# Kernel optimization log

Hardware: AMD Instinct MI355X
Metric: run time of the kernel (lower is better)

Reference implementation:

```python
import jax, jax.numpy as jnp
import numpy as np

B, S, K, D = 2, 2048, 8, 1024
P, KP, DFF = 32, 4, 4096


def setup_inputs() -> dict:
    key = jax.random.key(0)
    ks = jax.random.split(key, 17)
    s = 0.02
    return {
        "x": jax.random.normal(ks[0], (B, S, D), jnp.float32),
        "router_out": jax.random.normal(ks[1], (B, S, D), jnp.float32),
        "topk_neuron_idx": jax.random.randint(ks[2], (B, S, K), 0, 512, jnp.int32),
        "topk_neuron_weights": jax.random.uniform(ks[3], (B, S, K), jnp.float32),
        "selected_neurons": jax.random.normal(ks[4], (B, S, K, D), jnp.float32),
        "context": jax.random.normal(ks[5], (B, S, D), jnp.float32),
        "Wq": jax.random.normal(ks[6], (D, D), jnp.float32) * s,
        "bq": jnp.zeros((D,), jnp.float32),
        "Wk": jax.random.normal(ks[7], (D, D), jnp.float32) * s,
        "bk": jnp.zeros((D,), jnp.float32),
        "Wv": jax.random.normal(ks[8], (D, D), jnp.float32) * s,
        "bv": jnp.zeros((D,), jnp.float32),
        "pattern_queries": jax.random.normal(ks[9], (P, D), jnp.float32) * s,
        "Wup": jax.random.normal(ks[10], (DFF, D), jnp.float32) * s,
        "bup": jnp.zeros((DFF,), jnp.float32),
        "Wdown": jax.random.normal(ks[11], (D, DFF), jnp.float32) * s,
        "bdown": jnp.zeros((D,), jnp.float32),
    }


def reference(x, router_out, topk_neuron_idx, topk_neuron_weights,
              selected_neurons, context, Wq, bq, Wk, bk, Wv, bv,
              pattern_queries, Wup, bup, Wdown, bdown):
    scale = 1.0 / jnp.sqrt(jnp.float32(D))
    # K-wide neuron self-attention (per token), torch Linear: y = x @ W.T + b
    q = jnp.einsum('bskd,ed->bske', selected_neurons, Wq) + bq
    kk = jnp.einsum('bskd,ed->bske', selected_neurons, Wk) + bk
    v = jnp.einsum('bskd,ed->bske', selected_neurons, Wv) + bv
    attn = jax.nn.softmax(jnp.einsum('bsqd,bskd->bsqk', q, kk) * scale, axis=-1)
    interacted = jnp.einsum('bsqk,bskd->bsqd', attn, v)  # [B,S,K,D]
    # pattern similarity: [B,S,P,K]
    nps = jnp.einsum('pd,bskd->bspk', pattern_queries, interacted) * scale
    neuron_based = (nps * topk_neuron_weights[:, :, None, :]).sum(-1)  # [B,S,P]
    context_based = jnp.einsum('bsd,pd->bsp', context, pattern_queries)
    pattern_scores = 0.5 * neuron_based + 0.5 * context_based
    topk_scores, topk_idx = jax.lax.top_k(pattern_scores, KP)  # [B,S,KP]
    topk_w = jax.nn.softmax(topk_scores, axis=-1)
    sel_attn = jnp.take_along_axis(nps, topk_idx[..., None], axis=2)  # [B,S,KP,K]
    final_attn = (topk_w[..., None] * jax.nn.softmax(sel_attn, axis=-1)).sum(2)  # [B,S,K]
    aggregated = jnp.einsum('bsk,bskd->bsd', final_attn, interacted)
    combined = x + aggregated
    h = jax.nn.gelu(combined @ Wup.T + bup, approximate=False)
    return h @ Wdown.T + bdown
```

## Files before the change

kernel.cpp:

```cpp
#include <hip/hip_runtime.h>
#include <math.h>

typedef unsigned short ushort_t;
typedef __attribute__((ext_vector_type(8))) short short8;
typedef __attribute__((ext_vector_type(4))) float floatx4;

static __device__ __forceinline__ ushort_t f2bf(float f){
  unsigned int u = __float_as_uint(f);
  unsigned int r = u + 0x7FFFu + ((u >> 16) & 1u);
  return (ushort_t)(r >> 16);
}
static __device__ __forceinline__ void unpack8(uint4 u, float* f){
  f[0] = __uint_as_float(u.x << 16); f[1] = __uint_as_float(u.x & 0xffff0000u);
  f[2] = __uint_as_float(u.y << 16); f[3] = __uint_as_float(u.y & 0xffff0000u);
  f[4] = __uint_as_float(u.z << 16); f[5] = __uint_as_float(u.z & 0xffff0000u);
  f[6] = __uint_as_float(u.w << 16); f[7] = __uint_as_float(u.w & 0xffff0000u);
}
static __device__ __forceinline__ uint4 pack8(const float* f){
  uint4 u;
  u.x = (unsigned)f2bf(f[0]) | ((unsigned)f2bf(f[1]) << 16);
  u.y = (unsigned)f2bf(f[2]) | ((unsigned)f2bf(f[3]) << 16);
  u.z = (unsigned)f2bf(f[4]) | ((unsigned)f2bf(f[5]) << 16);
  u.w = (unsigned)f2bf(f[6]) | ((unsigned)f2bf(f[7]) << 16);
  return u;
}

static __device__ __forceinline__ void gload16(const void* g, void* l){
  __builtin_amdgcn_global_load_lds((const __attribute__((address_space(1))) void*)g,
                                   (__attribute__((address_space(3))) void*)l, 16, 0, 0);
}

__global__ __launch_bounds__(256) void k_cvt_multi(
    const float* __restrict__ s0, ushort_t* __restrict__ d0, int e0,
    const float* __restrict__ s1, ushort_t* __restrict__ d1, int e1,
    const float* __restrict__ s2, ushort_t* __restrict__ d2, int e2,
    const float* __restrict__ s3, ushort_t* __restrict__ d3, int e3,
    const float* __restrict__ s4, ushort_t* __restrict__ d4, int e4,
    const float* __restrict__ s5, ushort_t* __restrict__ d5, int e5){
  int i = blockIdx.x * 256 + threadIdx.x;
  const float* s; ushort_t* d; int b;
  if      (i < e0){ s = s0; d = d0; b = 0;  }
  else if (i < e1){ s = s1; d = d1; b = e0; }
  else if (i < e2){ s = s2; d = d2; b = e1; }
  else if (i < e3){ s = s3; d = d3; b = e2; }
  else if (i < e4){ s = s4; d = d4; b = e3; }
  else if (i < e5){ s = s5; d = d5; b = e4; }
  else return;
  int j = i - b;
  float4 v = ((const float4*)s)[j];
  unsigned long long p = (unsigned long long)f2bf(v.x)
                       | ((unsigned long long)f2bf(v.y) << 16)
                       | ((unsigned long long)f2bf(v.z) << 32)
                       | ((unsigned long long)f2bf(v.w) << 48);
  ((unsigned long long*)d)[j] = p;
}

__global__ __launch_bounds__(256) void k_transpose3(const float* __restrict__ s0, ushort_t* __restrict__ d0,
                                                    const float* __restrict__ s1, ushort_t* __restrict__ d1,
                                                    const float* __restrict__ s2, ushort_t* __restrict__ d2){
  __shared__ float tile[32][33];
  const float* in; ushort_t* out;
  if      (blockIdx.z == 0){ in = s0; out = d0; }
  else if (blockIdx.z == 1){ in = s1; out = d1; }
  else                     { in = s2; out = d2; }
  int bx = blockIdx.x * 32, by = blockIdx.y * 32;
  int tx = threadIdx.x & 31, ty = threadIdx.x >> 5;
  for (int i = 0; i < 32; i += 8)
    tile[ty + i][tx] = in[(size_t)(by + ty + i) * 1024 + bx + tx];
  __syncthreads();
  for (int i = 0; i < 32; i += 8)
    out[(size_t)(bx + ty + i) * 1024 + by + tx] = f2bf(tile[tx][ty + i]);
}

__global__ __launch_bounds__(256) void k_prep(const float* __restrict__ bq,
                                              const ushort_t* __restrict__ WKT,
                                              float* __restrict__ wv,
                                              const float* __restrict__ pat,
                                              const float* __restrict__ bv,
                                              float* __restrict__ pb,
                                              const ushort_t* __restrict__ WVT,
                                              const ushort_t* __restrict__ PATB,
                                              ushort_t* __restrict__ PVB){
  const int bid = blockIdx.x;
  const int l = threadIdx.x & 63;
  if (bid < 256){
    int d = (bid << 2) + (threadIdx.x >> 6);
    const uint4* row = (const uint4*)(WKT + (size_t)d * 1024 + (l << 4));
    const float4* b4 = (const float4*)(bq + (l << 4));
    float w[16], bb[16];
    unpack8(row[0], w); unpack8(row[1], w + 8);
#pragma unroll
    for (int i = 0; i < 4; i++){
      float4 v = b4[i];
      bb[i*4] = v.x; bb[i*4+1] = v.y; bb[i*4+2] = v.z; bb[i*4+3] = v.w;
    }
    float a = 0.f;
#pragma unroll
    for (int i = 0; i < 16; i++) a += w[i] * bb[i];
#pragma unroll
    for (int s = 1; s < 64; s <<= 1) a += __shfl_xor(a, s);
    if (l == 0) wv[d] = a;
  } else if (bid < 264){
    int p = ((bid - 256) << 2) + (threadIdx.x >> 6);
    const float4* pr = (const float4*)(pat + p * 1024) + l;
    const float4* b4 = (const float4*)bv + l;
    float a = 0.f;
#pragma unroll
    for (int i = 0; i < 4; i++){
      float4 x = pr[i * 64], y = b4[i * 64];
      a += x.x * y.x + x.y * y.y + x.z * y.z + x.w * y.w;
    }
#pragma unroll
    for (int s = 1; s < 64; s <<= 1) a += __shfl_xor(a, s);
    if (l == 0) pb[p] = a;
  } else {
    int d = ((bid - 264) << 2) + (threadIdx.x >> 6);
    const uint4* wr = (const uint4*)(WVT + (size_t)d * 1024 + (l << 4));
    float w[16];
    unpack8(wr[0], w); unpack8(wr[1], w + 8);
    for (int p = 0; p < 32; p++){
      const uint4* pr = (const uint4*)(PATB + p * 1024 + (l << 4));
      float pw[16];
      unpack8(pr[0], pw); unpack8(pr[1], pw + 8);
      float a = 0.f;
#pragma unroll
      for (int i = 0; i < 16; i++) a += w[i] * pw[i];
#pragma unroll
      for (int s = 1; s < 64; s <<= 1) a += __shfl_xor(a, s);
      if (l == 0) PVB[p * 1024 + d] = f2bf(a);
    }
  }
}

template<int MODE, int GN>
__global__ __launch_bounds__(256) void k_gemm_bt(const ushort_t* __restrict__ A,
                                                 const ushort_t* __restrict__ B,
                                                 void* __restrict__ C,
                                                 const float* __restrict__ bias,
                                                 const float* __restrict__ Xadd,
                                                 int N, int K){
  __shared__ ushort_t As[128 * 32];
  __shared__ ushort_t Bs[128 * 32];
  const int tid = threadIdx.x;
  const int w = tid >> 6, l = tid & 63;
  const int id = blockIdx.x;
  const int xcd = id & 7;
  const int t2 = id >> 3;
  const int nt = t2 % GN;
  const int mt = ((t2 / GN) << 3) + xcd;
  const int m0 = mt << 7, n0 = nt << 7;
  const int wm = (w >> 1) << 6, wn = (w & 1) << 6;
  const int rA = (w << 4) + (l >> 2);
  const int cA = (l & 3) << 3;
  const int fr = l & 15, fq = l >> 4;

  floatx4 acc[4][4];
#pragma unroll
  for (int i = 0; i < 4; i++)
#pragma unroll
    for (int j = 0; j < 4; j++) acc[i][j] = (floatx4)0.0f;

  const ushort_t* Ab = A + (size_t)(m0 + rA) * K + cA;
  const ushort_t* Bb = B + (size_t)(n0 + rA) * K + cA;
  const size_t row64 = (size_t)64 * K;
  ushort_t* Asw = As + (w << 9);
  ushort_t* Bsw = Bs + (w << 9);

  for (int k0 = 0; k0 < K; k0 += 32){
    __syncthreads();
    gload16(Ab + k0, Asw);
    gload16(Ab + row64 + k0, Asw + 2048);
    gload16(Bb + k0, Bsw);
    gload16(Bb + row64 + k0, Bsw + 2048);
    __syncthreads();
    short8 af[4], bg[4];
#pragma unroll
    for (int i = 0; i < 4; i++){
      af[i] = *(const short8*)(As + ((wm + (i << 4) + fr) << 5) + (fq << 3));
      bg[i] = *(const short8*)(Bs + ((wn + (i << 4) + fr) << 5) + (fq << 3));
    }
#pragma unroll
    for (int i = 0; i < 4; i++)
#pragma unroll
      for (int j = 0; j < 4; j++)
        acc[i][j] = __builtin_amdgcn_mfma_f32_16x16x32_bf16(af[i], bg[j], acc[i][j], 0, 0, 0);
  }

#pragma unroll
  for (int i = 0; i < 4; i++){
    int row = m0 + wm + (i << 4) + (fq << 2);
#pragma unroll
    for (int j = 0; j < 4; j++){
      int col = n0 + wn + (j << 4) + fr;
      float b = (MODE >= 1) ? bias[col] : 0.0f;
#pragma unroll
      for (int r = 0; r < 4; r++){
        float v = acc[i][j][r] + b;
        size_t idx = (size_t)(row + r) * N + col;
        if (MODE == 2) v += Xadd[idx];
        if (MODE == 3) v = 0.5f * v * (1.0f + erff(v * 0.70710678118654752f));
        if (MODE == 4) ((float*)C)[idx] = v;
        else           ((ushort_t*)C)[idx] = f2bf(v);
      }
    }
  }
}

template<int MODE, int GN>
__global__ __launch_bounds__(256) void k_gemm_bt64(const ushort_t* __restrict__ A,
                                                   const ushort_t* __restrict__ B,
                                                   void* __restrict__ C,
                                                   const float* __restrict__ bias,
                                                   const float* __restrict__ Xadd,
                                                   int N, int K){
  __shared__ ushort_t As[64 * 32];
  __shared__ ushort_t Bs[128 * 32];
  const int tid = threadIdx.x;
  const int w = tid >> 6, l = tid & 63;
  const int id = blockIdx.x;
  const int xcd = id & 7;
  const int t2 = id >> 3;
  const int nt = t2 % GN;
  const int mt = ((t2 / GN) << 3) + xcd;
  const int m0 = mt << 6, n0 = nt << 7;
  const int wm = (w >> 1) << 5, wn = (w & 1) << 6;
  const int rA = (w << 4) + (l >> 2);
  const int cA = (l & 3) << 3;
  const int fr = l & 15, fq = l >> 4;

  floatx4 acc[2][4];
#pragma unroll
  for (int i = 0; i < 2; i++)
#pragma unroll
    for (int j = 0; j < 4; j++) acc[i][j] = (floatx4)0.0f;

  const ushort_t* Ab = A + (size_t)(m0 + rA) * K + cA;
  const ushort_t* Bb = B + (size_t)(n0 + rA) * K + cA;
  const size_t row64 = (size_t)64 * K;

  for (int k0 = 0; k0 < K; k0 += 32){
    __syncthreads();
    gload16(Ab + k0, As + (w << 9));
    gload16(Bb + k0, Bs + (w << 9));
    gload16(Bb + row64 + k0, Bs + 2048 + (w << 9));
    __syncthreads();
    short8 af[2], bg[4];
#pragma unroll
    for (int i = 0; i < 2; i++)
      af[i] = *(const short8*)(As + ((wm + (i << 4) + fr) << 5) + (fq << 3));
#pragma unroll
    for (int j = 0; j < 4; j++)
      bg[j] = *(const short8*)(Bs + ((wn + (j << 4) + fr) << 5) + (fq << 3));
#pragma unroll
    for (int i = 0; i < 2; i++)
#pragma unroll
      for (int j = 0; j < 4; j++)
        acc[i][j] = __builtin_amdgcn_mfma_f32_16x16x32_bf16(af[i], bg[j], acc[i][j], 0, 0, 0);
  }

#pragma unroll
  for (int i = 0; i < 2; i++){
    int row = m0 + wm + (i << 4) + (fq << 2);
#pragma unroll
    for (int j = 0; j < 4; j++){
      int col = n0 + wn + (j << 4) + fr;
      float b = (MODE >= 1) ? bias[col] : 0.0f;
#pragma unroll
      for (int r = 0; r < 4; r++){
        float v = acc[i][j][r] + b;
        size_t idx = (size_t)(row + r) * N + col;
        if (MODE == 2) v += Xadd[idx];
        if (MODE == 3) v = 0.5f * v * (1.0f + erff(v * 0.70710678118654752f));
        if (MODE == 4) ((float*)C)[idx] = v;
        else           ((ushort_t*)C)[idx] = f2bf(v);
      }
    }
  }
}

__global__ __launch_bounds__(256) void k_gemm_n32(const ushort_t* __restrict__ A,
                                                  const ushort_t* __restrict__ B,
                                                  float* __restrict__ C,
                                                  int K){
  __shared__ ushort_t As[128 * 32];
  __shared__ ushort_t Bs[32 * 32];
  const int tid = threadIdx.x;
  const int w = tid >> 6, l = tid & 63;
  const int m0 = blockIdx.x << 7;
  const int rA = (w << 4) + (l >> 2);
  const int cA = (l & 3) << 3;
  const int fr = l & 15, fq = l >> 4;

  floatx4 acc[2][2];
#pragma unroll
  for (int i = 0; i < 2; i++)
#pragma unroll
    for (int j = 0; j < 2; j++) acc[i][j] = (floatx4)0.0f;

  const ushort_t* Ab = A + (size_t)(m0 + rA) * K + cA;
  const ushort_t* Bb = B + (size_t)rA * K + cA;
  const size_t row64 = (size_t)64 * K;

  for (int k0 = 0; k0 < K; k0 += 32){
    __syncthreads();
    gload16(Ab + k0, As + (w << 9));
    gload16(Ab + row64 + k0, As + 2048 + (w << 9));
    if (w < 2) gload16(Bb + k0, Bs + (w << 9));
    __syncthreads();
    short8 af[2], bg[2];
#pragma unroll
    for (int i = 0; i < 2; i++)
      af[i] = *(const short8*)(As + (((w << 5) + (i << 4) + fr) << 5) + (fq << 3));
#pragma unroll
    for (int j = 0; j < 2; j++)
      bg[j] = *(const short8*)(Bs + (((j << 4) + fr) << 5) + (fq << 3));
#pragma unroll
    for (int i = 0; i < 2; i++)
#pragma unroll
      for (int j = 0; j < 2; j++)
        acc[i][j] = __builtin_amdgcn_mfma_f32_16x16x32_bf16(af[i], bg[j], acc[i][j], 0, 0, 0);
  }

#pragma unroll
  for (int i = 0; i < 2; i++){
    int row = m0 + (w << 5) + (i << 4) + (fq << 2);
#pragma unroll
    for (int j = 0; j < 2; j++){
      int col = (j << 4) + fr;
#pragma unroll
      for (int r = 0; r < 4; r++)
        C[(size_t)(row + r) * 32 + col] = acc[i][j][r];
    }
  }
}

__global__ __launch_bounds__(256) void k_attn(const ushort_t* __restrict__ T,
                                              const ushort_t* __restrict__ SNB,
                                              const ushort_t* __restrict__ PVB,
                                              const float* __restrict__ PBv,
                                              const float* __restrict__ CB,
                                              const float* __restrict__ TW,
                                              ushort_t* __restrict__ GSN){
  __shared__ float logit_s[4 * 256];
  __shared__ float attn_s[8 * 64];
  __shared__ float npr_s[8 * 256];
  __shared__ float nps_s[8 * 256];
  __shared__ float sc_s[8 * 32];
  __shared__ float tw_s[8 * 8];
  __shared__ float pb_s[32];
  __shared__ int   sel_s[8 * 4];
  __shared__ float tkw_s[8 * 4], rmax_s[8 * 4], rsum_s[8 * 4], fa_s[8 * 8], g_s[8 * 8];

  const int t = threadIdx.x;
  const int w = t >> 6, l = t & 63;
  const int tok0 = blockIdx.x << 3;
  const int pair = (blockIdx.x << 2) + w;

  {
    const size_t rbase = (size_t)pair * 16 + (l & 15);
    const int ko = (l >> 4) << 3;
    const ushort_t* Ap = T   + rbase * 1024 + ko;
    const ushort_t* Bp = SNB + rbase * 1024 + ko;
    const ushort_t* P0 = PVB + (size_t)(l & 15) * 1024 + ko;
    const ushort_t* P1 = P0 + 16 * 1024;
    floatx4 aL = (floatx4)0.0f, aP0 = (floatx4)0.0f, aP1 = (floatx4)0.0f;
#pragma unroll 4
    for (int k0 = 0; k0 < 1024; k0 += 32){
      short8 b = *(const short8*)(Bp + k0);
      aL  = __builtin_amdgcn_mfma_f32_16x16x32_bf16(*(const short8*)(Ap + k0), b, aL, 0, 0, 0);
      aP0 = __builtin_amdgcn_mfma_f32_16x16x32_bf16(*(const short8*)(P0 + k0), b, aP0, 0, 0, 0);
      aP1 = __builtin_amdgcn_mfma_f32_16x16x32_bf16(*(const short8*)(P1 + k0), b, aP1, 0, 0, 0);
    }
    const int col = l & 15, r0 = (l >> 4) << 2;
#pragma unroll
    for (int r = 0; r < 4; r++)
      logit_s[(w << 8) + (r0 + r) * 16 + col] = aL[r] * 0.03125f;
    const int tokloc = (w << 1) + (col >> 3), kk = col & 7;
#pragma unroll
    for (int r = 0; r < 4; r++){
      npr_s[(tokloc << 8) + kk * 32 + (r0 + r)]      = aP0[r];
      npr_s[(tokloc << 8) + kk * 32 + (r0 + r) + 16] = aP1[r];
    }
  }
  if (t < 64) tw_s[t] = TW[(tok0 << 3) + t];
  if (t < 32) pb_s[t] = PBv[t];
  __syncthreads();

  const int loc = t >> 5, q = t & 31;
  if (q < 8){
    const float* lrow = logit_s + ((loc >> 1) << 8) + (loc & 1) * 136 + q * 16;
    float a[8]; float m = -1e30f;
#pragma unroll
    for (int j = 0; j < 8; j++){ a[j] = lrow[j]; m = fmaxf(m, a[j]); }
    float s = 0.f;
#pragma unroll
    for (int j = 0; j < 8; j++){ a[j] = expf(a[j] - m); s += a[j]; }
    float inv = 1.f / s;
#pragma unroll
    for (int j = 0; j < 8; j++) attn_s[(loc << 6) + q * 8 + j] = a[j] * inv;
  }
  __syncthreads();

  {
    const int qq = q & 7, p0 = (q >> 3) << 3;
    float a[8];
#pragma unroll
    for (int k = 0; k < 8; k++) a[k] = attn_s[(loc << 6) + qq * 8 + k];
    const float* np = npr_s + (loc << 8);
    float* npsr = nps_s + (loc << 8);
    for (int p = p0; p < p0 + 8; p++){
      float acc = pb_s[p];
#pragma unroll
      for (int k = 0; k < 8; k++) acc += a[k] * np[k * 32 + p];
      npsr[p * 8 + qq] = acc * 0.03125f;
    }
  }
  __syncthreads();

  {
    const float* npsr = nps_s + (loc << 8);
    float nb = 0.f;
#pragma unroll
    for (int qq = 0; qq < 8; qq++) nb += npsr[q * 8 + qq] * tw_s[(loc << 3) + qq];
    sc_s[(loc << 5) + q] = 0.5f * nb + 0.5f * CB[((size_t)(tok0 + loc) << 5) + q];
  }
  __syncthreads();

  if (q == 0){
    const float* sc = sc_s + (loc << 5);
    unsigned used = 0; float vals[4]; int idx[4];
    for (int kp = 0; kp < 4; kp++){
      float best = -1e30f; int bi = 0;
      for (int p = 0; p < 32; p++)
        if (!((used >> p) & 1u) && sc[p] > best){ best = sc[p]; bi = p; }
      used |= 1u << bi; vals[kp] = best; idx[kp] = bi;
    }
    float mm = vals[0], ss = 0.f, e[4];
    for (int kp = 0; kp < 4; kp++){ e[kp] = expf(vals[kp] - mm); ss += e[kp]; }
    for (int kp = 0; kp < 4; kp++){ tkw_s[(loc << 2) + kp] = e[kp] / ss; sel_s[(loc << 2) + kp] = idx[kp]; }
  }
  __syncthreads();

  if (q < 4){
    const float* npsr = nps_s + (loc << 8);
    int p = sel_s[(loc << 2) + q];
    float mm = -1e30f;
    for (int j = 0; j < 8; j++) mm = fmaxf(mm, npsr[p * 8 + j]);
    float ss = 0.f;
    for (int j = 0; j < 8; j++) ss += expf(npsr[p * 8 + j] - mm);
    rmax_s[(loc << 2) + q] = mm; rsum_s[(loc << 2) + q] = ss;
  }
  __syncthreads();

  if (q < 8){
    const float* npsr = nps_s + (loc << 8);
    float f = 0.f;
    for (int kp = 0; kp < 4; kp++){
      int p = sel_s[(loc << 2) + kp];
      f += tkw_s[(loc << 2) + kp] * expf(npsr[p * 8 + q] - rmax_s[(loc << 2) + kp]) / rsum_s[(loc << 2) + kp];
    }
    fa_s[(loc << 3) + q] = f;
  }
  __syncthreads();

  if (q < 8){
    float g = 0.f;
    for (int qq = 0; qq < 8; qq++) g += fa_s[(loc << 3) + qq] * attn_s[(loc << 6) + qq * 8 + q];
    g_s[(loc << 3) + q] = g;
  }
  __syncthreads();

  for (int tl = 0; tl < 2; tl++){
    const int tkl = (w << 1) + tl;
    const size_t tok = (size_t)tok0 + tkl;
    float o[16];
#pragma unroll
    for (int i = 0; i < 16; i++) o[i] = 0.f;
#pragma unroll
    for (int k = 0; k < 8; k++){
      float gk = g_s[(tkl << 3) + k];
      const uint4* src = (const uint4*)(SNB + ((tok << 3) + k) * 1024 + (l << 4));
      float f0[8], f1[8];
      unpack8(src[0], f0);
      unpack8(src[1], f1);
#pragma unroll
      for (int i = 0; i < 8; i++){ o[i] += gk * f0[i]; o[8 + i] += gk * f1[i]; }
    }
    uint4* dst = (uint4*)(GSN + tok * 1024 + (l << 4));
    dst[0] = pack8(o);
    dst[1] = pack8(o + 8);
  }
}

extern "C" void kernel_launch(void* const* d_in, const int* in_sizes, int n_in,
                              void* d_out, int out_size, void* d_ws, size_t ws_size,
                              hipStream_t stream){
  (void)in_sizes; (void)n_in; (void)out_size; (void)ws_size;
  const float* x   = (const float*)d_in[0];
  const float* tw  = (const float*)d_in[3];
  const float* SN  = (const float*)d_in[4];
  const float* ctx = (const float*)d_in[5];
  const float* Wq  = (const float*)d_in[6];
  const float* bq  = (const float*)d_in[7];
  const float* Wk  = (const float*)d_in[8];
  const float* Wv  = (const float*)d_in[10];
  const float* bv  = (const float*)d_in[11];
  const float* pat = (const float*)d_in[12];
  const float* Wup = (const float*)d_in[13];
  const float* bup = (const float*)d_in[14];
  const float* Wdn = (const float*)d_in[15];
  const float* bdn = (const float*)d_in[16];
  float* out = (float*)d_out;

  char* ws = (char*)d_ws;
  size_t off = 0;
  auto alloc = [&](size_t bytes) -> char* {
    char* p = ws + off;
    off = (off + bytes + 255) & ~(size_t)255;
    return p;
  };
  ushort_t* SNB  = (ushort_t*)alloc(67108864);
  ushort_t* TB   = (ushort_t*)alloc(67108864);
  float*    CBb  = (float*)alloc(524288);
  ushort_t* GSN  = (ushort_t*)alloc(8388608);
  ushort_t* CTXB = (ushort_t*)alloc(8388608);
  ushort_t* PATB = (ushort_t*)alloc(65536);
  ushort_t* WVB  = (ushort_t*)alloc(2097152);
  ushort_t* WUPB = (ushort_t*)alloc(8388608);
  ushort_t* WDNB = (ushort_t*)alloc(8388608);
  ushort_t* ATB  = (ushort_t*)alloc(2097152);
  ushort_t* WKTB = (ushort_t*)alloc(2097152);
  ushort_t* WQTB = (ushort_t*)alloc(2097152);
  ushort_t* WVTB = (ushort_t*)alloc(2097152);
  ushort_t* PVB  = (ushort_t*)alloc(65536);
  float*    WVEC = (float*)alloc(4096);
  float*    PBv  = (float*)alloc(128);
  ushort_t* H    = SNB;
  ushort_t* CMB  = TB;

  const int e0 = 8388608, e1 = e0 + 1048576, e2 = e1 + 8192,
            e3 = e2 + 262144, e4 = e3 + 1048576, e5 = e4 + 1048576;
  k_cvt_multi<<<(e5 + 255) / 256, 256, 0, stream>>>(
      SN, SNB, e0, ctx, CTXB, e1, pat, PATB, e2,
      Wv, WVB, e3, Wup, WUPB, e4, Wdn, WDNB, e5);
  k_transpose3<<<dim3(32, 32, 3), 256, 0, stream>>>(Wq, WQTB, Wk, WKTB, Wv, WVTB);
  k_prep<<<520, 256, 0, stream>>>(bq, WKTB, WVEC, pat, bv, PBv, WVTB, PATB, PVB);

  k_gemm_bt64<0, 8><<<128, 256, 0, stream>>>(WKTB, WQTB, ATB, nullptr, nullptr, 1024, 1024);
  k_gemm_bt<1, 8><<<2048, 256, 0, stream>>>(SNB, ATB, TB, WVEC, nullptr, 1024, 1024);
  k_gemm_n32<<<32, 256, 0, stream>>>(CTXB, PATB, CBb, 1024);
  k_attn<<<512, 256, 0, stream>>>(TB, SNB, PVB, PBv, CBb, tw, GSN);
  k_gemm_bt64<2, 8><<<512, 256, 0, stream>>>(GSN, WVB, CMB, bv, x, 1024, 1024);
  k_gemm_bt<3, 32><<<1024, 256, 0, stream>>>(CMB, WUPB, H, bup, nullptr, 4096, 1024);
  k_gemm_bt64<4, 8><<<512, 256, 0, stream>>>(H, WDNB, out, bdn, nullptr, 1024, 4096);
}
```

Baseline: 630.5 us.

## Split-K down projection with atomics, grouped tile order, and tanh-form GELU

The down-projection GEMM is split over K into two halves that atomically accumulate into an fp32 output. That output is pre-initialised with the bias inside the conversion kernel. Block-to-tile mapping in the 128-tile GEMM is regrouped so that consecutive blocks share N-tile groups, which should improve L2 reuse. The exact erf GELU is replaced by a sigmoid/tanh-form approximation using __expf, trading accuracy for cheaper math, and the atomics add contention and nondeterministic summation order.

```diff
diff --git a/kernel.cpp b/kernel.cpp
--- a/kernel.cpp
+++ b/kernel.cpp
@@ -30,22 +30,34 @@
                                    (__attribute__((address_space(3))) void*)l, 16, 0, 0);
 }
 
+static __device__ __forceinline__ float gelu_f(float v){
+  float w = v * (-1.5957691216f - 0.0713548162f * v * v);
+  return v / (1.0f + __expf(w));
+}
+
 __global__ __launch_bounds__(256) void k_cvt_multi(
     const float* __restrict__ s0, ushort_t* __restrict__ d0, int e0,
     const float* __restrict__ s1, ushort_t* __restrict__ d1, int e1,
     const float* __restrict__ s2, ushort_t* __restrict__ d2, int e2,
     const float* __restrict__ s3, ushort_t* __restrict__ d3, int e3,
     const float* __restrict__ s4, ushort_t* __restrict__ d4, int e4,
-    const float* __restrict__ s5, ushort_t* __restrict__ d5, int e5){
+    const float* __restrict__ s5, ushort_t* __restrict__ d5, int e5,
+    const float* __restrict__ bdn, float* __restrict__ outp, int e6){
   int i = blockIdx.x * 256 + threadIdx.x;
+  if (i >= e5){
+    if (i < e6){
+      int j = i - e5;
+      ((float4*)outp)[j] = ((const float4*)bdn)[j & 255];
+    }
+    return;
+  }
   const float* s; ushort_t* d; int b;
   if      (i < e0){ s = s0; d = d0; b = 0;  }
   else if (i < e1){ s = s1; d = d1; b = e0; }
   else if (i < e2){ s = s2; d = d2; b = e1; }
   else if (i < e3){ s = s3; d = d3; b = e2; }
   else if (i < e4){ s = s4; d = d4; b = e3; }
-  else if (i < e5){ s = s5; d = d5; b = e4; }
-  else return;
+  else            { s = s5; d = d5; b = e4; }
   int j = i - b;
   float4 v = ((const float4*)s)[j];
   unsigned long long p = (unsigned long long)f2bf(v.x)
@@ -132,7 +144,7 @@
   }
 }
 
-template<int MODE, int GN>
+template<int MODE, int GN, int NG>
 __global__ __launch_bounds__(256) void k_gemm_bt(const ushort_t* __restrict__ A,
                                                  const ushort_t* __restrict__ B,
                                                  void* __restrict__ C,
@@ -146,8 +158,12 @@
   const int id = blockIdx.x;
   const int xcd = id & 7;
   const int t2 = id >> 3;
-  const int nt = t2 % GN;
-  const int mt = ((t2 / GN) << 3) + xcd;
+  const int nmq = (int)(gridDim.x >> 3) / GN;
+  const int gsz = nmq * NG;
+  const int g = t2 / gsz, r = t2 - g * gsz;
+  const int mq = r / NG, nw = r - mq * NG;
+  const int nt = g * NG + nw;
+  const int mt = (mq << 3) + xcd;
   const int m0 = mt << 7, n0 = nt << 7;
   const int wm = (w >> 1) << 6, wn = (w & 1) << 6;
   const int rA = (w << 4) + (l >> 2);
@@ -194,11 +210,11 @@
       int col = n0 + wn + (j << 4) + fr;
       float b = (MODE >= 1) ? bias[col] : 0.0f;
 #pragma unroll
-      for (int r = 0; r < 4; r++){
-        float v = acc[i][j][r] + b;
-        size_t idx = (size_t)(row + r) * N + col;
+      for (int r2 = 0; r2 < 4; r2++){
+        float v = acc[i][j][r2] + b;
+        size_t idx = (size_t)(row + r2) * N + col;
         if (MODE == 2) v += Xadd[idx];
-        if (MODE == 3) v = 0.5f * v * (1.0f + erff(v * 0.70710678118654752f));
+        if (MODE == 3) v = gelu_f(v);
         if (MODE == 4) ((float*)C)[idx] = v;
         else           ((ushort_t*)C)[idx] = f2bf(v);
       }
@@ -206,7 +222,7 @@
   }
 }
 
-template<int MODE, int GN>
+template<int MODE, int GN, int KS>
 __global__ __launch_bounds__(256) void k_gemm_bt64(const ushort_t* __restrict__ A,
                                                    const ushort_t* __restrict__ B,
                                                    void* __restrict__ C,
@@ -220,9 +236,13 @@
   const int id = blockIdx.x;
   const int xcd = id & 7;
   const int t2 = id >> 3;
-  const int nt = t2 % GN;
-  const int mt = ((t2 / GN) << 3) + xcd;
+  const int nmq = (int)(gridDim.x >> 3) / (GN * KS);
+  const int nt = t2 / (nmq * KS);
+  const int r2 = t2 - nt * (nmq * KS);
+  const int mq = r2 / KS, kh = r2 - mq * KS;
+  const int mt = (mq << 3) + xcd;
   const int m0 = mt << 6, n0 = nt << 7;
+  const int kbase = kh * (K / KS);
   const int wm = (w >> 1) << 5, wn = (w & 1) << 6;
   const int rA = (w << 4) + (l >> 2);
   const int cA = (l & 3) << 3;
@@ -234,11 +254,12 @@
 #pragma unroll
     for (int j = 0; j < 4; j++) acc[i][j] = (floatx4)0.0f;
 
-  const ushort_t* Ab = A + (size_t)(m0 + rA) * K + cA;
-  const ushort_t* Bb = B + (size_t)(n0 + rA) * K + cA;
+  const ushort_t* Ab = A + (size_t)(m0 + rA) * K + cA + kbase;
+  const ushort_t* Bb = B + (size_t)(n0 + rA) * K + cA + kbase;
   const size_t row64 = (size_t)64 * K;
-
-  for (int k0 = 0; k0 < K; k0 += 32){
+  const int klen = K / KS;
+
+  for (int k0 = 0; k0 < klen; k0 += 32){
     __syncthreads();
     gload16(Ab + k0, As + (w << 9));
     gload16(Bb + k0, Bs + (w << 9));
@@ -264,14 +285,13 @@
 #pragma unroll
     for (int j = 0; j < 4; j++){
       int col = n0 + wn + (j << 4) + fr;
-      float b = (MODE >= 1) ? bias[col] : 0.0f;
+      float b = (MODE == 2) ? bias[col] : 0.0f;
 #pragma unroll
       for (int r = 0; r < 4; r++){
         float v = acc[i][j][r] + b;
         size_t idx = (size_t)(row + r) * N + col;
         if (MODE == 2) v += Xadd[idx];
-        if (MODE == 3) v = 0.5f * v * (1.0f + erff(v * 0.70710678118654752f));
-        if (MODE == 4) ((float*)C)[idx] = v;
+        if (MODE == 5) atomicAdd(((float*)C) + idx, v);
         else           ((ushort_t*)C)[idx] = f2bf(v);
       }
     }
@@ -539,18 +559,19 @@
   ushort_t* CMB  = TB;
 
   const int e0 = 8388608, e1 = e0 + 1048576, e2 = e1 + 8192,
-            e3 = e2 + 262144, e4 = e3 + 1048576, e5 = e4 + 1048576;
-  k_cvt_multi<<<(e5 + 255) / 256, 256, 0, stream>>>(
+            e3 = e2 + 262144, e4 = e3 + 1048576, e5 = e4 + 1048576,
+            e6 = e5 + 1048576;
+  k_cvt_multi<<<(e6 + 255) / 256, 256, 0, stream>>>(
       SN, SNB, e0, ctx, CTXB, e1, pat, PATB, e2,
-      Wv, WVB, e3, Wup, WUPB, e4, Wdn, WDNB, e5);
+      Wv, WVB, e3, Wup, WUPB, e4, Wdn, WDNB, e5, bdn, out, e6);
   k_transpose3<<<dim3(32, 32, 3), 256, 0, stream>>>(Wq, WQTB, Wk, WKTB, Wv, WVTB);
   k_prep<<<520, 256, 0, stream>>>(bq, WKTB, WVEC, pat, bv, PBv, WVTB, PATB, PVB);
 
-  k_gemm_bt64<0, 8><<<128, 256, 0, stream>>>(WKTB, WQTB, ATB, nullptr, nullptr, 1024, 1024);
-  k_gemm_bt<1, 8><<<2048, 256, 0, stream>>>(SNB, ATB, TB, WVEC, nullptr, 1024, 1024);
+  k_gemm_bt64<0, 8, 1><<<128, 256, 0, stream>>>(WKTB, WQTB, ATB, nullptr, nullptr, 1024, 1024);
+  k_gemm_bt<1, 8, 8><<<2048, 256, 0, stream>>>(SNB, ATB, TB, WVEC, nullptr, 1024, 1024);
   k_gemm_n32<<<32, 256, 0, stream>>>(CTXB, PATB, CBb, 1024);
   k_attn<<<512, 256, 0, stream>>>(TB, SNB, PVB, PBv, CBb, tw, GSN);
-  k_gemm_bt64<2, 8><<<512, 256, 0, stream>>>(GSN, WVB, CMB, bv, x, 1024, 1024);
-  k_gemm_bt<3, 32><<<1024, 256, 0, stream>>>(CMB, WUPB, H, bup, nullptr, 4096, 1024);
-  k_gemm_bt64<4, 8><<<512, 256, 0, stream>>>(H, WDNB, out, bdn, nullptr, 1024, 4096);
-}
+  k_gemm_bt64<2, 8, 1><<<512, 256, 0, stream>>>(GSN, WVB, CMB, bv, x, 1024, 1024);
+  k_gemm_bt<3, 32, 4><<<1024, 256, 0, stream>>>(CMB, WUPB, H, bup, nullptr, 4096, 1024);
+  k_gemm_bt64<5, 8, 2><<<1024, 256, 0, stream>>>(H, WDNB, out, nullptr, nullptr, 1024, 4096);
+}
```

New measurement: 630.3 us. About the same (-0.0%).

## Double GEMM K-step, group tile order, fuse ctx GEMM into prep, fast GELU

Applied to the files above, without the earlier changes.

GEMM kernels now stage 64-wide K slices per barrier pair instead of 32, halving synchronisation count at the cost of doubled LDS. Block-to-tile mapping is regrouped so neighbouring blocks share N tiles for better L2 reuse. The small context×pattern GEMM is folded into the prep kernel as extra blocks, removing a launch. Exact erf GELU is replaced by a sigmoid-based tanh approximation, trading accuracy for fewer instructions.

```diff
diff --git a/kernel.cpp b/kernel.cpp
--- a/kernel.cpp
+++ b/kernel.cpp
@@ -28,6 +28,11 @@
 static __device__ __forceinline__ void gload16(const void* g, void* l){
   __builtin_amdgcn_global_load_lds((const __attribute__((address_space(1))) void*)g,
                                    (__attribute__((address_space(3))) void*)l, 16, 0, 0);
+}
+
+static __device__ __forceinline__ float gelu_f(float v){
+  float w = v * (-1.5957691216f - 0.0713548162f * v * v);
+  return v / (1.0f + __expf(w));
 }
 
 __global__ __launch_bounds__(256) void k_cvt_multi(
@@ -80,7 +85,11 @@
                                               float* __restrict__ pb,
                                               const ushort_t* __restrict__ WVT,
                                               const ushort_t* __restrict__ PATB,
-                                              ushort_t* __restrict__ PVB){
+                                              ushort_t* __restrict__ PVB,
+                                              const ushort_t* __restrict__ CTXB,
+                                              float* __restrict__ CBb){
+  __shared__ ushort_t As[128 * 32];
+  __shared__ ushort_t Bs[32 * 32];
   const int bid = blockIdx.x;
   const int l = threadIdx.x & 63;
   if (bid < 256){
@@ -113,7 +122,7 @@
 #pragma unroll
     for (int s = 1; s < 64; s <<= 1) a += __shfl_xor(a, s);
     if (l == 0) pb[p] = a;
-  } else {
+  } else if (bid < 520){
     int d = ((bid - 264) << 2) + (threadIdx.x >> 6);
     const uint4* wr = (const uint4*)(WVT + (size_t)d * 1024 + (l << 4));
     float w[16];
@@ -129,25 +138,75 @@
       for (int s = 1; s < 64; s <<= 1) a += __shfl_xor(a, s);
       if (l == 0) PVB[p * 1024 + d] = f2bf(a);
     }
-  }
-}
-
-template<int MODE, int GN>
+  } else {
+    const int tid = threadIdx.x;
+    const int w = tid >> 6;
+    const int m0 = (bid - 520) << 7;
+    const int rA = (w << 4) + (l >> 2);
+    const int cA = (l & 3) << 3;
+    const int fr = l & 15, fq = l >> 4;
+    const int K = 1024;
+    floatx4 acc[2][2];
+#pragma unroll
+    for (int i = 0; i < 2; i++)
+#pragma unroll
+      for (int j = 0; j < 2; j++) acc[i][j] = (floatx4)0.0f;
+    const ushort_t* Ab = CTXB + (size_t)(m0 + rA) * K + cA;
+    const ushort_t* Bb = PATB + (size_t)rA * K + cA;
+    const size_t row64 = (size_t)64 * K;
+    for (int k0 = 0; k0 < K; k0 += 32){
+      __syncthreads();
+      gload16(Ab + k0, As + (w << 9));
+      gload16(Ab + row64 + k0, As + 2048 + (w << 9));
+      if (w < 2) gload16(Bb + k0, Bs + (w << 9));
+      __syncthreads();
+      short8 af[2], bg[2];
+#pragma unroll
+      for (int i = 0; i < 2; i++)
+        af[i] = *(const short8*)(As + (((w << 5) + (i << 4) + fr) << 5) + (fq << 3));
+#pragma unroll
+      for (int j = 0; j < 2; j++)
+        bg[j] = *(const short8*)(Bs + (((j << 4) + fr) << 5) + (fq << 3));
+#pragma unroll
+      for (int i = 0; i < 2; i++)
+#pragma unroll
+        for (int j = 0; j < 2; j++)
+          acc[i][j] = __builtin_amdgcn_mfma_f32_16x16x32_bf16(af[i], bg[j], acc[i][j], 0, 0, 0);
+    }
+#pragma unroll
+    for (int i = 0; i < 2; i++){
+      int row = m0 + (w << 5) + (i << 4) + (fq << 2);
+#pragma unroll
+      for (int j = 0; j < 2; j++){
+        int col = (j << 4) + fr;
+#pragma unroll
+        for (int r = 0; r < 4; r++)
+          CBb[(size_t)(row + r) * 32 + col] = acc[i][j][r];
+      }
+    }
+  }
+}
+
+template<int MODE, int GN, int NG>
 __global__ __launch_bounds__(256) void k_gemm_bt(const ushort_t* __restrict__ A,
                                                  const ushort_t* __restrict__ B,
                                                  void* __restrict__ C,
                                                  const float* __restrict__ bias,
                                                  const float* __restrict__ Xadd,
                                                  int N, int K){
-  __shared__ ushort_t As[128 * 32];
-  __shared__ ushort_t Bs[128 * 32];
+  __shared__ ushort_t As[2 * 128 * 32];
+  __shared__ ushort_t Bs[2 * 128 * 32];
   const int tid = threadIdx.x;
   const int w = tid >> 6, l = tid & 63;
   const int id = blockIdx.x;
   const int xcd = id & 7;
   const int t2 = id >> 3;
-  const int nt = t2 % GN;
-  const int mt = ((t2 / GN) << 3) + xcd;
+  const int nmq = (int)(gridDim.x >> 3) / GN;
+  const int gsz = nmq * NG;
+  const int g = t2 / gsz, r = t2 - g * gsz;
+  const int mq = r / NG, nw = r - mq * NG;
+  const int nt = g * NG + nw;
+  const int mt = (mq << 3) + xcd;
   const int m0 = mt << 7, n0 = nt << 7;
   const int wm = (w >> 1) << 6, wn = (w & 1) << 6;
   const int rA = (w << 4) + (l >> 2);
@@ -166,24 +225,33 @@
   ushort_t* Asw = As + (w << 9);
   ushort_t* Bsw = Bs + (w << 9);
 
-  for (int k0 = 0; k0 < K; k0 += 32){
+  for (int k0 = 0; k0 < K; k0 += 64){
     __syncthreads();
     gload16(Ab + k0, Asw);
     gload16(Ab + row64 + k0, Asw + 2048);
+    gload16(Ab + k0 + 32, Asw + 4096);
+    gload16(Ab + row64 + k0 + 32, Asw + 6144);
     gload16(Bb + k0, Bsw);
     gload16(Bb + row64 + k0, Bsw + 2048);
+    gload16(Bb + k0 + 32, Bsw + 4096);
+    gload16(Bb + row64 + k0 + 32, Bsw + 6144);
     __syncthreads();
-    short8 af[4], bg[4];
-#pragma unroll
-    for (int i = 0; i < 4; i++){
-      af[i] = *(const short8*)(As + ((wm + (i << 4) + fr) << 5) + (fq << 3));
-      bg[i] = *(const short8*)(Bs + ((wn + (i << 4) + fr) << 5) + (fq << 3));
-    }
-#pragma unroll
-    for (int i = 0; i < 4; i++)
-#pragma unroll
-      for (int j = 0; j < 4; j++)
-        acc[i][j] = __builtin_amdgcn_mfma_f32_16x16x32_bf16(af[i], bg[j], acc[i][j], 0, 0, 0);
+#pragma unroll
+    for (int h = 0; h < 2; h++){
+      const ushort_t* Ah = As + (h << 12);
+      const ushort_t* Bh = Bs + (h << 12);
+      short8 af[4], bg[4];
+#pragma unroll
+      for (int i = 0; i < 4; i++){
+        af[i] = *(const short8*)(Ah + ((wm + (i << 4) + fr) << 5) + (fq << 3));
+        bg[i] = *(const short8*)(Bh + ((wn + (i << 4) + fr) << 5) + (fq << 3));
+      }
+#pragma unroll
+      for (int i = 0; i < 4; i++)
+#pragma unroll
+        for (int j = 0; j < 4; j++)
+          acc[i][j] = __builtin_amdgcn_mfma_f32_16x16x32_bf16(af[i], bg[j], acc[i][j], 0, 0, 0);
+    }
   }
 
 #pragma unroll
@@ -194,11 +262,11 @@
       int col = n0 + wn + (j << 4) + fr;
       float b = (MODE >= 1) ? bias[col] : 0.0f;
 #pragma unroll
-      for (int r = 0; r < 4; r++){
-        float v = acc[i][j][r] + b;
-        size_t idx = (size_t)(row + r) * N + col;
+      for (int r2 = 0; r2 < 4; r2++){
+        float v = acc[i][j][r2] + b;
+        size_t idx = (size_t)(row + r2) * N + col;
         if (MODE == 2) v += Xadd[idx];
-        if (MODE == 3) v = 0.5f * v * (1.0f + erff(v * 0.70710678118654752f));
+        if (MODE == 3) v = gelu_f(v);
         if (MODE == 4) ((float*)C)[idx] = v;
         else           ((ushort_t*)C)[idx] = f2bf(v);
       }
@@ -213,15 +281,17 @@
                                                    const float* __restrict__ bias,
                                                    const float* __restrict__ Xadd,
                                                    int N, int K){
-  __shared__ ushort_t As[64 * 32];
-  __shared__ ushort_t Bs[128 * 32];
+  __shared__ ushort_t As[2 * 64 * 32];
+  __shared__ ushort_t Bs[2 * 128 * 32];
   const int tid = threadIdx.x;
   const int w = tid >> 6, l = tid & 63;
   const int id = blockIdx.x;
   const int xcd = id & 7;
   const int t2 = id >> 3;
-  const int nt = t2 % GN;
-  const int mt = ((t2 / GN) << 3) + xcd;
+  const int nmq = (int)(gridDim.x >> 3) / GN;
+  const int nt = t2 / nmq;
+  const int mq = t2 - nt * nmq;
+  const int mt = (mq << 3) + xcd;
   const int m0 = mt << 6, n0 = nt << 7;
   const int wm = (w >> 1) << 5, wn = (w & 1) << 6;
   const int rA = (w << 4) + (l >> 2);
@@ -238,24 +308,32 @@
   const ushort_t* Bb = B + (size_t)(n0 + rA) * K + cA;
   const size_t row64 = (size_t)64 * K;
 
-  for (int k0 = 0; k0 < K; k0 += 32){
+  for (int k0 = 0; k0 < K; k0 += 64){
     __syncthreads();
     gload16(Ab + k0, As + (w << 9));
+    gload16(Ab + k0 + 32, As + 2048 + (w << 9));
     gload16(Bb + k0, Bs + (w << 9));
     gload16(Bb + row64 + k0, Bs + 2048 + (w << 9));
+    gload16(Bb + k0 + 32, Bs + 4096 + (w << 9));
+    gload16(Bb + row64 + k0 + 32, Bs + 6144 + (w << 9));
     __syncthreads();
-    short8 af[2], bg[4];
-#pragma unroll
-    for (int i = 0; i < 2; i++)
-      af[i] = *(const short8*)(As + ((wm + (i << 4) + fr) << 5) + (fq << 3));
-#pragma unroll
-    for (int j = 0; j < 4; j++)
-      bg[j] = *(const short8*)(Bs + ((wn + (j << 4) + fr) << 5) + (fq << 3));
-#pragma unroll
-    for (int i = 0; i < 2; i++)
+#pragma unroll
+    for (int h = 0; h < 2; h++){
+      const ushort_t* Ah = As + (h << 11);
+      const ushort_t* Bh = Bs + (h << 12);
+      short8 af[2], bg[4];
+#pragma unroll
+      for (int i = 0; i < 2; i++)
+        af[i] = *(const short8*)(Ah + ((wm + (i << 4) + fr) << 5) + (fq << 3));
 #pragma unroll
       for (int j = 0; j < 4; j++)
-        acc[i][j] = __builtin_amdgcn_mfma_f32_16x16x32_bf16(af[i], bg[j], acc[i][j], 0, 0, 0);
+        bg[j] = *(const short8*)(Bh + ((wn + (j << 4) + fr) << 5) + (fq << 3));
+#pragma unroll
+      for (int i = 0; i < 2; i++)
+#pragma unroll
+        for (int j = 0; j < 4; j++)
+          acc[i][j] = __builtin_amdgcn_mfma_f32_16x16x32_bf16(af[i], bg[j], acc[i][j], 0, 0, 0);
+    }
   }
 
 #pragma unroll
@@ -264,72 +342,15 @@
 #pragma unroll
     for (int j = 0; j < 4; j++){
       int col = n0 + wn + (j << 4) + fr;
-      float b = (MODE >= 1) ? bias[col] : 0.0f;
+      float b = (MODE >= 2) ? bias[col] : 0.0f;
 #pragma unroll
       for (int r = 0; r < 4; r++){
         float v = acc[i][j][r] + b;
         size_t idx = (size_t)(row + r) * N + col;
         if (MODE == 2) v += Xadd[idx];
-        if (MODE == 3) v = 0.5f * v * (1.0f + erff(v * 0.70710678118654752f));
         if (MODE == 4) ((float*)C)[idx] = v;
         else           ((ushort_t*)C)[idx] = f2bf(v);
       }
-    }
-  }
-}
-
-__global__ __launch_bounds__(256) void k_gemm_n32(const ushort_t* __restrict__ A,
-                                                  const ushort_t* __restrict__ B,
-                                                  float* __restrict__ C,
-                                                  int K){
-  __shared__ ushort_t As[128 * 32];
-  __shared__ ushort_t Bs[32 * 32];
-  const int tid = threadIdx.x;
-  const int w = tid >> 6, l = tid & 63;
-  const int m0 = blockIdx.x << 7;
-  const int rA = (w << 4) + (l >> 2);
-  const int cA = (l & 3) << 3;
-  const int fr = l & 15, fq = l >> 4;
-
-  floatx4 acc[2][2];
-#pragma unroll
-  for (int i = 0; i < 2; i++)
-#pragma unroll
-    for (int j = 0; j < 2; j++) acc[i][j] = (floatx4)0.0f;
-
-  const ushort_t* Ab = A + (size_t)(m0 + rA) * K + cA;
-  const ushort_t* Bb = B + (size_t)rA * K + cA;
-  const size_t row64 = (size_t)64 * K;
-
-  for (int k0 = 0; k0 < K; k0 += 32){
-    __syncthreads();
-    gload16(Ab + k0, As + (w << 9));
-    gload16(Ab + row64 + k0, As + 2048 + (w << 9));
-    if (w < 2) gload16(Bb + k0, Bs + (w << 9));
-    __syncthreads();
-    short8 af[2], bg[2];
-#pragma unroll
-    for (int i = 0; i < 2; i++)
-      af[i] = *(const short8*)(As + (((w << 5) + (i << 4) + fr) << 5) + (fq << 3));
-#pragma unroll
-    for (int j = 0; j < 2; j++)
-      bg[j] = *(const short8*)(Bs + (((j << 4) + fr) << 5) + (fq << 3));
-#pragma unroll
-    for (int i = 0; i < 2; i++)
-#pragma unroll
-      for (int j = 0; j < 2; j++)
-        acc[i][j] = __builtin_amdgcn_mfma_f32_16x16x32_bf16(af[i], bg[j], acc[i][j], 0, 0, 0);
-  }
-
-#pragma unroll
-  for (int i = 0; i < 2; i++){
-    int row = m0 + (w << 5) + (i << 4) + (fq << 2);
-#pragma unroll
-    for (int j = 0; j < 2; j++){
-      int col = (j << 4) + fr;
-#pragma unroll
-      for (int r = 0; r < 4; r++)
-        C[(size_t)(row + r) * 32 + col] = acc[i][j][r];
     }
   }
 }
@@ -544,13 +565,12 @@
       SN, SNB, e0, ctx, CTXB, e1, pat, PATB, e2,
       Wv, WVB, e3, Wup, WUPB, e4, Wdn, WDNB, e5);
   k_transpose3<<<dim3(32, 32, 3), 256, 0, stream>>>(Wq, WQTB, Wk, WKTB, Wv, WVTB);
-  k_prep<<<520, 256, 0, stream>>>(bq, WKTB, WVEC, pat, bv, PBv, WVTB, PATB, PVB);
+  k_prep<<<552, 256, 0, stream>>>(bq, WKTB, WVEC, pat, bv, PBv, WVTB, PATB, PVB, CTXB, CBb);
 
   k_gemm_bt64<0, 8><<<128, 256, 0, stream>>>(WKTB, WQTB, ATB, nullptr, nullptr, 1024, 1024);
-  k_gemm_bt<1, 8><<<2048, 256, 0, stream>>>(SNB, ATB, TB, WVEC, nullptr, 1024, 1024);
-  k_gemm_n32<<<32, 256, 0, stream>>>(CTXB, PATB, CBb, 1024);
+  k_gemm_bt<1, 8, 8><<<2048, 256, 0, stream>>>(SNB, ATB, TB, WVEC, nullptr, 1024, 1024);
   k_attn<<<512, 256, 0, stream>>>(TB, SNB, PVB, PBv, CBb, tw, GSN);
   k_gemm_bt64<2, 8><<<512, 256, 0, stream>>>(GSN, WVB, CMB, bv, x, 1024, 1024);
-  k_gemm_bt<3, 32><<<1024, 256, 0, stream>>>(CMB, WUPB, H, bup, nullptr, 4096, 1024);
+  k_gemm_bt<3, 32, 4><<<1024, 256, 0, stream>>>(CMB, WUPB, H, bup, nullptr, 4096, 1024);
   k_gemm_bt64<4, 8><<<512, 256, 0, stream>>>(H, WDNB, out, bdn, nullptr, 1024, 4096);
 }
```

Measured after the change: 585.0 us. 1.08x faster.
